# Kernel tuning notes

Hardware: AMD Instinct MI355X
Metric: run time of the kernel (lower is better)

The kernel has to match this reference:

```python
import jax, jax.numpy as jnp
import numpy as np
import math

NUM_WORDS = 8192
WORD_WIDTH = 512
PROJ_WIDTH = 64
NUM_HEADS = 8
SCALE_FACTOR = 100.0

def setup_inputs() -> dict:
    key = jax.random.key(0)
    kx, kq, kk, kv, ko = jax.random.split(key, 5)
    x = jax.random.normal(kx, (NUM_WORDS, WORD_WIDTH), dtype=jnp.float32)
    w_q = jax.random.normal(kq, (WORD_WIDTH, PROJ_WIDTH), dtype=jnp.float32) / SCALE_FACTOR
    w_k = jax.random.normal(kk, (WORD_WIDTH, PROJ_WIDTH), dtype=jnp.float32) / SCALE_FACTOR
    w_v = jax.random.normal(kv, (WORD_WIDTH, PROJ_WIDTH), dtype=jnp.float32) / SCALE_FACTOR
    w_o = jax.random.normal(ko, (WORD_WIDTH, WORD_WIDTH), dtype=jnp.float32)
    return {"x": x, "w_q": w_q, "w_k": w_k, "w_v": w_v, "w_o": w_o}

def reference(x, w_q, w_k, w_v, w_o):
    # Single self-attention head (all 8 heads in the source share the same weights).
    q = x @ w_q            # [N, P]
    k = x @ w_k            # [N, P]
    v = x @ w_v            # [N, P]
    scores = jax.nn.softmax((q @ k.T) / jnp.sqrt(jnp.float32(q.shape[1])), axis=1)  # [N, N]
    head = scores @ v      # [N, P]
    # concat of NUM_HEADS identical head outputs along dim=1
    concat = jnp.tile(head, (1, NUM_HEADS))  # [N, NUM_HEADS*P]
    return concat @ w_o    # [N, WORD_WIDTH]
```

## Files before the change

kernel.cpp:

```cpp
#include <hip/hip_runtime.h>
#include <stdint.h>

#define N_WORDS 8192
#define LOG2E_8 0.18033688011112043f

typedef __attribute__((ext_vector_type(8))) short short8;
typedef __attribute__((ext_vector_type(4))) float f32x4;
typedef __attribute__((ext_vector_type(16))) float f32x16;
typedef __attribute__((ext_vector_type(2))) __fp16 pkhalf2;
typedef __attribute__((ext_vector_type(4))) _Float16 half4;
typedef __attribute__((ext_vector_type(8))) _Float16 half8;

__device__ __forceinline__ unsigned short f32_to_bf16(float f) {
    union { float f; unsigned u; } v; v.f = f;
    unsigned u = v.u;
    return (unsigned short)((u + 0x7FFFu + ((u >> 16) & 1u)) >> 16);
}

__device__ __forceinline__ unsigned short f32_to_f16(float f) {
    union { _Float16 h; unsigned short u; } cv;
    cv.h = (_Float16)f;
    return cv.u;
}

__device__ __forceinline__ void async16(const void* g, void* l) {
    __builtin_amdgcn_global_load_lds(
        (const __attribute__((address_space(1))) unsigned int*)g,
        (__attribute__((address_space(3))) unsigned int*)l, 16, 0, 0);
}

__global__ __launch_bounds__(256) void qkv_gemm(
    const float* __restrict__ x,
    const float* __restrict__ wq, const float* __restrict__ wk,
    const float* __restrict__ wv, const float* __restrict__ wo,
    unsigned short* __restrict__ qB, unsigned short* __restrict__ kB,
    unsigned short* __restrict__ vH, unsigned short* __restrict__ weT)
{
    int t = threadIdx.x;
    int mat = blockIdx.y;

    if (mat == 3) {
        int i = blockIdx.x * 256 + t;
        int p = i >> 9;
        int j = i & 511;
        float s = 0.0f;
#pragma unroll
        for (int h = 0; h < 8; ++h) s += wo[(size_t)(h * 64 + p) * 512 + j];
        weT[(size_t)j * 64 + p] = f32_to_f16(s);
        return;
    }

    __shared__ __align__(16) unsigned short ldsX[64 * 72];
    __shared__ __align__(16) unsigned short ldsW[64 * 72];

    int mt = blockIdx.x;
    const float* w = (mat == 0) ? wq : (mat == 1) ? wk : wv;

    int wvid = t >> 6, lane = t & 63;
    int lq = lane & 15, quad = lane >> 4;

    f32x4 acc[4];
#pragma unroll
    for (int nt = 0; nt < 4; ++nt) acc[nt] = (f32x4){0.f, 0.f, 0.f, 0.f};

    float4 xr[4];
    float wr[16];
    int wn = t & 63, wkbs = (t >> 6) * 16;

    {
#pragma unroll
        for (int j2 = 0; j2 < 4; ++j2) {
            int i = t + j2 * 256;
            int row = i >> 4, c4 = (i & 15) * 4;
            xr[j2] = *(const float4*)(x + (size_t)(mt * 64 + row) * 512 + c4);
        }
#pragma unroll
        for (int kk = 0; kk < 16; ++kk)
            wr[kk] = w[(size_t)(wkbs + kk) * 64 + wn];
    }

    for (int kb = 0; kb < 8; ++kb) {
        __syncthreads();
#pragma unroll
        for (int j2 = 0; j2 < 4; ++j2) {
            int i = t + j2 * 256;
            int row = i >> 4, c4 = (i & 15) * 4;
            unsigned p0 = f32_to_bf16(xr[j2].x) | ((unsigned)f32_to_bf16(xr[j2].y) << 16);
            unsigned p1 = f32_to_bf16(xr[j2].z) | ((unsigned)f32_to_bf16(xr[j2].w) << 16);
            *(uint2*)(&ldsX[row * 72 + c4]) = make_uint2(p0, p1);
        }
#pragma unroll
        for (int kk = 0; kk < 16; kk += 2) {
            unsigned p = f32_to_bf16(wr[kk]) | ((unsigned)f32_to_bf16(wr[kk + 1]) << 16);
            *(unsigned*)(&ldsW[wn * 72 + wkbs + kk]) = p;
        }
        __syncthreads();

        if (kb < 7) {
            int k0 = (kb + 1) * 64;
#pragma unroll
            for (int j2 = 0; j2 < 4; ++j2) {
                int i = t + j2 * 256;
                int row = i >> 4, c4 = (i & 15) * 4;
                xr[j2] = *(const float4*)(x + (size_t)(mt * 64 + row) * 512 + k0 + c4);
            }
#pragma unroll
            for (int kk = 0; kk < 16; ++kk)
                wr[kk] = w[(size_t)(k0 + wkbs + kk) * 64 + wn];
        }

        int m = wvid * 16 + lq;
        short8 a0 = *(const short8*)(&ldsX[m * 72 + quad * 8]);
        short8 a1 = *(const short8*)(&ldsX[m * 72 + 32 + quad * 8]);
#pragma unroll
        for (int nt = 0; nt < 4; ++nt) {
            short8 b0 = *(const short8*)(&ldsW[(nt * 16 + lq) * 72 + quad * 8]);
            short8 b1 = *(const short8*)(&ldsW[(nt * 16 + lq) * 72 + 32 + quad * 8]);
            acc[nt] = __builtin_amdgcn_mfma_f32_16x16x32_bf16(a0, b0, acc[nt], 0, 0, 0);
            acc[nt] = __builtin_amdgcn_mfma_f32_16x16x32_bf16(a1, b1, acc[nt], 0, 0, 0);
        }
    }

    __syncthreads();
    unsigned short* ldsO = ldsX;
#pragma unroll
    for (int nt = 0; nt < 4; ++nt) {
#pragma unroll
        for (int r = 0; r < 4; ++r) {
            int lr = wvid * 16 + quad * 4 + r;
            int n = nt * 16 + lq;
            float v = acc[nt][r];
            int off;
            unsigned short u;
            if (mat == 0) {
                v *= LOG2E_8;
                int col = (((n >> 3) ^ (lr & 7)) << 3) | (n & 7);
                off = lr * 64 + col;
                u = f32_to_bf16(v);
            } else if (mat == 1) {
                int c2 = n >> 3, j = n & 7;
                off = (((lr >> 5) << 2) + (c2 >> 1)) * 512
                    + (((c2 & 1) << 5) + (lr & 31)) * 8 + j;
                u = f32_to_bf16(v);
            } else {
                int j2 = (lr & 3) | (((lr >> 3) & 1) << 2);
                off = ((((lr >> 5) << 1) + ((lr >> 4) & 1)) * 2 + (n >> 5)) * 512
                    + ((((lr >> 2) & 1) << 5) + (n & 31)) * 8 + j2;
                u = f32_to_f16(v);
            }
            ldsO[off] = u;
        }
    }
    __syncthreads();
    {
        unsigned short* dst = (mat == 0) ? qB : (mat == 1) ? kB : vH;
        const uint4* U = (const uint4*)ldsO;
        uint4* G = (uint4*)((char*)dst + (size_t)mt * 8192);
        G[t] = U[t];
        G[t + 256] = U[t + 256];
    }
}

__global__ __launch_bounds__(512, 2) void attn_kernel(
    const unsigned short* __restrict__ qB,
    const unsigned short* __restrict__ kB,
    const unsigned short* __restrict__ vH,
    unsigned short* __restrict__ pOh, float* __restrict__ pl,
    int nk, int sshift)
{
    __shared__ __align__(16) unsigned short ldsK[4][128 * 64];
    __shared__ __align__(16) unsigned short ldsV[4][64 * 128];

    int t = threadIdx.x;
    int bid = blockIdx.x;
    int s = bid & ((1 << sshift) - 1);
    int qb = bid >> sshift;
    int wvid = t >> 6, lane = t & 63;
    int l31 = lane & 31, hi = lane >> 5;
    int mbase = qb * 256 + wvid * 32;
    int n0 = s * nk;

    short8 qf[4];
    {
        int qrow = mbase + l31;
        const unsigned short* qr = qB + (size_t)qrow * 64;
        int s7 = qrow & 7;
#pragma unroll
        for (int c = 0; c < 4; ++c)
            qf[c] = *(const short8*)(qr + (((2 * c + hi) ^ s7) << 3));
    }

    f32x16 zero16;
#pragma unroll
    for (int i = 0; i < 16; ++i) zero16[i] = 0.f;
    f32x16 oacc[2];
    oacc[0] = zero16;
    oacc[1] = zero16;
    float lsum = 0.f;

    auto stage = [&](int ti, int nb) {
        int buf = ti & 3;
        const char* gK = (const char*)kB + (size_t)(nb >> 7) * 16384;
        const char* gV = (const char*)vH + (size_t)(nb >> 7) * 16384;
        async16(gK + ((size_t)(wvid * 64) + lane) * 16,
                (char*)ldsK[buf] + (size_t)wvid * 1024);
        async16(gK + ((size_t)(512 + wvid * 64) + lane) * 16,
                (char*)ldsK[buf] + 8192 + (size_t)wvid * 1024);
        async16(gV + ((size_t)(wvid * 64) + lane) * 16,
                (char*)ldsV[buf] + (size_t)wvid * 1024);
        async16(gV + ((size_t)(512 + wvid * 64) + lane) * 16,
                (char*)ldsV[buf] + 8192 + (size_t)wvid * 1024);
    };

    int tiles = nk >> 7;
    stage(0, n0);
    stage(1, n0 + 128);
    stage(2, n0 + 256);

    for (int tt = 0; tt < tiles; ++tt) {
        int rem = tiles - 1 - tt;
        if (rem >= 2)      asm volatile("s_waitcnt vmcnt(8)" ::: "memory");
        else if (rem == 1) asm volatile("s_waitcnt vmcnt(4)" ::: "memory");
        else               asm volatile("s_waitcnt vmcnt(0)" ::: "memory");
        __builtin_amdgcn_sched_barrier(0);
        __builtin_amdgcn_s_barrier();
        __builtin_amdgcn_sched_barrier(0);

        if (tt + 3 < tiles) stage(tt + 3, n0 + (tt + 3) * 128);

        __builtin_amdgcn_s_setprio(1);
        const char* Kb = (const char*)ldsK[tt & 3] + (size_t)lane * 16;
        const char* Vb = (const char*)ldsV[tt & 3] + (size_t)lane * 16;

#pragma unroll
        for (int nt = 0; nt < 4; ++nt) {
            f32x16 st = zero16;
#pragma unroll
            for (int c = 0; c < 4; ++c) {
                short8 a = *(const short8*)(Kb + (nt * 4 + c) * 1024);
                st = __builtin_amdgcn_mfma_f32_32x32x16_bf16(a, qf[c], st, 0, 0, 0);
            }

            union { half8 v8[2]; pkhalf2 v2[8]; } pa;
#pragma unroll
            for (int p = 0; p < 8; ++p) {
                float e0 = exp2f(st[2 * p]);
                float e1 = exp2f(st[2 * p + 1]);
                lsum += e0 + e1;
                pa.v2[p] = __builtin_amdgcn_cvt_pkrtz(e0, e1);
            }

#pragma unroll
            for (int m = 0; m < 2; ++m) {
#pragma unroll
                for (int vt = 0; vt < 2; ++vt) {
                    half8 vb = *(const half8*)(Vb + (((nt * 2 + m) * 2) + vt) * 1024);
                    oacc[vt] = __builtin_amdgcn_mfma_f32_32x32x16_f16(
                        pa.v8[m], vb, oacc[vt], 0, 0, 0);
                }
            }
        }
        __builtin_amdgcn_s_setprio(0);
    }

    lsum += __shfl_xor(lsum, 32);

    size_t obase = (size_t)s * N_WORDS;
    if (hi == 0) pl[obase + mbase + l31] = lsum;

    __syncthreads();
    unsigned short* ldsO = &ldsK[0][0];
#pragma unroll
    for (int vt = 0; vt < 2; ++vt)
#pragma unroll
        for (int r = 0; r < 16; ++r) {
            int lrow = wvid * 32 + (r & 3) + 8 * (r >> 2) + 4 * hi;
            ldsO[lrow * 64 + vt * 32 + l31] = f32_to_f16(oacc[vt][r]);
        }
    __syncthreads();
    {
        const uint4* U = (const uint4*)ldsO;
        uint4* G = (uint4*)(pOh + (obase + (size_t)qb * 256) * 64);
#pragma unroll
        for (int j = 0; j < 4; ++j)
            G[t + 512 * j] = U[t + 512 * j];
    }
}

__global__ __launch_bounds__(256) void out_kernel(
    const unsigned short* __restrict__ pOh, const float* __restrict__ pl,
    const unsigned short* __restrict__ weT, float* __restrict__ out, int S)
{
    __shared__ __align__(16) _Float16 ldsH[16 * 72];
    int t = threadIdx.x;
    int r0 = blockIdx.x * 16;
    const _Float16* pOf = (const _Float16*)pOh;

#pragma unroll
    for (int j = 0; j < 4; ++j) {
        int i = t + j * 256;
        int row = i >> 6, d = i & 63;
        float so = 0.f, sl = 0.f;
        for (int s = 0; s < S; ++s) {
            so += (float)pOf[((size_t)s * N_WORDS + r0 + row) * 64 + d];
            sl += pl[(size_t)s * N_WORDS + r0 + row];
        }
        ldsH[row * 72 + d] = (_Float16)(so / sl);
    }
    __syncthreads();

    int wv = t >> 6, lane = t & 63;
    int lq = lane & 15, quad = lane >> 4;

    half8 a0 = *(const half8*)(&ldsH[lq * 72 + quad * 8]);
    half8 a1 = *(const half8*)(&ldsH[lq * 72 + 32 + quad * 8]);
    const _Float16* wT = (const _Float16*)weT;

#pragma unroll
    for (int ntl = 0; ntl < 8; ++ntl) {
        int nt = wv * 8 + ntl;
        const _Float16* wrow = wT + (size_t)(nt * 16 + lq) * 64;
        half8 b0 = *(const half8*)(wrow + quad * 8);
        half8 b1 = *(const half8*)(wrow + 32 + quad * 8);
        f32x4 acc = (f32x4){0.f, 0.f, 0.f, 0.f};
        acc = __builtin_amdgcn_mfma_f32_16x16x32_f16(a0, b0, acc, 0, 0, 0);
        acc = __builtin_amdgcn_mfma_f32_16x16x32_f16(a1, b1, acc, 0, 0, 0);
#pragma unroll
        for (int r = 0; r < 4; ++r)
            out[(size_t)(r0 + quad * 4 + r) * 512 + nt * 16 + lq] = acc[r];
    }
}

extern "C" void kernel_launch(void* const* d_in, const int* in_sizes, int n_in,
                              void* d_out, int out_size, void* d_ws, size_t ws_size,
                              hipStream_t stream)
{
    const float* x  = (const float*)d_in[0];
    const float* wq = (const float*)d_in[1];
    const float* wk = (const float*)d_in[2];
    const float* wv = (const float*)d_in[3];
    const float* wo = (const float*)d_in[4];
    float* out = (float*)d_out;

    char* ws = (char*)d_ws;
    unsigned short* qB  = (unsigned short*)(ws);
    unsigned short* kB  = (unsigned short*)(ws + 1048576);
    unsigned short* vH  = (unsigned short*)(ws + 2097152);
    unsigned short* weT = (unsigned short*)(ws + 3145728);
    float* pl           = (float*)(ws + 3211264);
    unsigned short* pOh = (unsigned short*)(ws + 3735552);

    size_t base = 3735552;
    int S = (ws_size >= base + 8u * 1048576u) ? 8 : 4;
    int sshift = (S == 8) ? 3 : 2;
    int nk = N_WORDS / S;
    int nqb = N_WORDS / 256;

    hipLaunchKernelGGL(qkv_gemm, dim3(128, 4), dim3(256), 0, stream,
                       x, wq, wk, wv, wo, qB, kB, vH, weT);
    hipLaunchKernelGGL(attn_kernel, dim3(nqb * S), dim3(512), 0, stream,
                       qB, kB, vH, pOh, pl, nk, sshift);
    hipLaunchKernelGGL(out_kernel, dim3(512), dim3(256), 0, stream,
                       pOh, pl, weT, out, S);
}
```

Baseline: 124.9 us.

## Fuse Q/K/V projections per block with 16-row tiles across 512 blocks

The QKV projection kernel now computes all three projections in one block over a 16-row tile of x, so each x tile is loaded and converted once instead of three times. The grid becomes 512 one-dimensional blocks instead of 128x4, and the w_o head-sum reduction is folded into the first 64 threads of each block. Output layouts are rewritten so the K and V tiled formats still match what the attention kernel expects. In exchange, every block reloads all three weight matrices, which raises weight traffic and register use.

```diff
diff --git a/kernel.cpp b/kernel.cpp
--- a/kernel.cpp
+++ b/kernel.cpp
@@ -36,100 +36,79 @@
     unsigned short* __restrict__ qB, unsigned short* __restrict__ kB,
     unsigned short* __restrict__ vH, unsigned short* __restrict__ weT)
 {
+    __shared__ __align__(16) unsigned short ldsX[16 * 72];
+    __shared__ __align__(16) unsigned short ldsW[3][64 * 72];
+
     int t = threadIdx.x;
-    int mat = blockIdx.y;
-
-    if (mat == 3) {
-        int i = blockIdx.x * 256 + t;
-        int p = i >> 9;
-        int j = i & 511;
-        float s = 0.0f;
-#pragma unroll
-        for (int h = 0; h < 8; ++h) s += wo[(size_t)(h * 64 + p) * 512 + j];
-        weT[(size_t)j * 64 + p] = f32_to_f16(s);
-        return;
-    }
-
-    __shared__ __align__(16) unsigned short ldsX[64 * 72];
-    __shared__ __align__(16) unsigned short ldsW[64 * 72];
-
     int mt = blockIdx.x;
-    const float* w = (mat == 0) ? wq : (mat == 1) ? wk : wv;
+    const float* wmat[3] = {wq, wk, wv};
 
     int wvid = t >> 6, lane = t & 63;
     int lq = lane & 15, quad = lane >> 4;
 
-    f32x4 acc[4];
-#pragma unroll
-    for (int nt = 0; nt < 4; ++nt) acc[nt] = (f32x4){0.f, 0.f, 0.f, 0.f};
-
-    float4 xr[4];
-    float wr[16];
+    f32x4 acc[3];
+#pragma unroll
+    for (int mat = 0; mat < 3; ++mat) acc[mat] = (f32x4){0.f, 0.f, 0.f, 0.f};
+
+    float4 xr;
+    float wr[3][16];
+    int xrow = t >> 4, xc4 = (t & 15) * 4;
     int wn = t & 63, wkbs = (t >> 6) * 16;
 
-    {
-#pragma unroll
-        for (int j2 = 0; j2 < 4; ++j2) {
-            int i = t + j2 * 256;
-            int row = i >> 4, c4 = (i & 15) * 4;
-            xr[j2] = *(const float4*)(x + (size_t)(mt * 64 + row) * 512 + c4);
-        }
+    xr = *(const float4*)(x + (size_t)(mt * 16 + xrow) * 512 + xc4);
+#pragma unroll
+    for (int mat = 0; mat < 3; ++mat)
 #pragma unroll
         for (int kk = 0; kk < 16; ++kk)
-            wr[kk] = w[(size_t)(wkbs + kk) * 64 + wn];
-    }
+            wr[mat][kk] = wmat[mat][(size_t)(wkbs + kk) * 64 + wn];
 
     for (int kb = 0; kb < 8; ++kb) {
         __syncthreads();
-#pragma unroll
-        for (int j2 = 0; j2 < 4; ++j2) {
-            int i = t + j2 * 256;
-            int row = i >> 4, c4 = (i & 15) * 4;
-            unsigned p0 = f32_to_bf16(xr[j2].x) | ((unsigned)f32_to_bf16(xr[j2].y) << 16);
-            unsigned p1 = f32_to_bf16(xr[j2].z) | ((unsigned)f32_to_bf16(xr[j2].w) << 16);
-            *(uint2*)(&ldsX[row * 72 + c4]) = make_uint2(p0, p1);
-        }
-#pragma unroll
-        for (int kk = 0; kk < 16; kk += 2) {
-            unsigned p = f32_to_bf16(wr[kk]) | ((unsigned)f32_to_bf16(wr[kk + 1]) << 16);
-            *(unsigned*)(&ldsW[wn * 72 + wkbs + kk]) = p;
-        }
+        {
+            unsigned p0 = f32_to_bf16(xr.x) | ((unsigned)f32_to_bf16(xr.y) << 16);
+            unsigned p1 = f32_to_bf16(xr.z) | ((unsigned)f32_to_bf16(xr.w) << 16);
+            *(uint2*)(&ldsX[xrow * 72 + xc4]) = make_uint2(p0, p1);
+        }
+#pragma unroll
+        for (int mat = 0; mat < 3; ++mat)
+#pragma unroll
+            for (int kk = 0; kk < 16; kk += 2) {
+                unsigned p = f32_to_bf16(wr[mat][kk]) |
+                             ((unsigned)f32_to_bf16(wr[mat][kk + 1]) << 16);
+                *(unsigned*)(&ldsW[mat][wn * 72 + wkbs + kk]) = p;
+            }
         __syncthreads();
 
         if (kb < 7) {
             int k0 = (kb + 1) * 64;
-#pragma unroll
-            for (int j2 = 0; j2 < 4; ++j2) {
-                int i = t + j2 * 256;
-                int row = i >> 4, c4 = (i & 15) * 4;
-                xr[j2] = *(const float4*)(x + (size_t)(mt * 64 + row) * 512 + k0 + c4);
-            }
-#pragma unroll
-            for (int kk = 0; kk < 16; ++kk)
-                wr[kk] = w[(size_t)(k0 + wkbs + kk) * 64 + wn];
-        }
-
-        int m = wvid * 16 + lq;
-        short8 a0 = *(const short8*)(&ldsX[m * 72 + quad * 8]);
-        short8 a1 = *(const short8*)(&ldsX[m * 72 + 32 + quad * 8]);
-#pragma unroll
-        for (int nt = 0; nt < 4; ++nt) {
-            short8 b0 = *(const short8*)(&ldsW[(nt * 16 + lq) * 72 + quad * 8]);
-            short8 b1 = *(const short8*)(&ldsW[(nt * 16 + lq) * 72 + 32 + quad * 8]);
-            acc[nt] = __builtin_amdgcn_mfma_f32_16x16x32_bf16(a0, b0, acc[nt], 0, 0, 0);
-            acc[nt] = __builtin_amdgcn_mfma_f32_16x16x32_bf16(a1, b1, acc[nt], 0, 0, 0);
-        }
-    }
-
-    __syncthreads();
-    unsigned short* ldsO = ldsX;
-#pragma unroll
-    for (int nt = 0; nt < 4; ++nt) {
+            xr = *(const float4*)(x + (size_t)(mt * 16 + xrow) * 512 + k0 + xc4);
+#pragma unroll
+            for (int mat = 0; mat < 3; ++mat)
+#pragma unroll
+                for (int kk = 0; kk < 16; ++kk)
+                    wr[mat][kk] = wmat[mat][(size_t)(k0 + wkbs + kk) * 64 + wn];
+        }
+
+        short8 a0 = *(const short8*)(&ldsX[lq * 72 + quad * 8]);
+        short8 a1 = *(const short8*)(&ldsX[lq * 72 + 32 + quad * 8]);
+#pragma unroll
+        for (int mat = 0; mat < 3; ++mat) {
+            short8 b0 = *(const short8*)(&ldsW[mat][(wvid * 16 + lq) * 72 + quad * 8]);
+            short8 b1 = *(const short8*)(&ldsW[mat][(wvid * 16 + lq) * 72 + 32 + quad * 8]);
+            acc[mat] = __builtin_amdgcn_mfma_f32_16x16x32_bf16(a0, b0, acc[mat], 0, 0, 0);
+            acc[mat] = __builtin_amdgcn_mfma_f32_16x16x32_bf16(a1, b1, acc[mat], 0, 0, 0);
+        }
+    }
+
+    __syncthreads();
+    unsigned short* ldsO = &ldsW[0][0];
+#pragma unroll
+    for (int mat = 0; mat < 3; ++mat) {
 #pragma unroll
         for (int r = 0; r < 4; ++r) {
-            int lr = wvid * 16 + quad * 4 + r;
-            int n = nt * 16 + lq;
-            float v = acc[nt][r];
+            int lr = quad * 4 + r;
+            int n = wvid * 16 + lq;
+            float v = acc[mat][r];
             int off;
             unsigned short u;
             if (mat == 0) {
@@ -139,13 +118,13 @@
                 u = f32_to_bf16(v);
             } else if (mat == 1) {
                 int c2 = n >> 3, j = n & 7;
-                off = (((lr >> 5) << 2) + (c2 >> 1)) * 512
-                    + (((c2 & 1) << 5) + (lr & 31)) * 8 + j;
+                off = 1024 + c2 * 128 + lr * 8 + j;
                 u = f32_to_bf16(v);
             } else {
                 int j2 = (lr & 3) | (((lr >> 3) & 1) << 2);
-                off = ((((lr >> 5) << 1) + ((lr >> 4) & 1)) * 2 + (n >> 5)) * 512
-                    + ((((lr >> 2) & 1) << 5) + (n & 31)) * 8 + j2;
+                int hi2 = (lr >> 2) & 1;
+                int vt = n >> 5;
+                off = 2048 + vt * 512 + ((hi2 << 5) + (n & 31)) * 8 + j2;
                 u = f32_to_f16(v);
             }
             ldsO[off] = u;
@@ -153,11 +132,26 @@
     }
     __syncthreads();
     {
-        unsigned short* dst = (mat == 0) ? qB : (mat == 1) ? kB : vH;
         const uint4* U = (const uint4*)ldsO;
-        uint4* G = (uint4*)((char*)dst + (size_t)mt * 8192);
-        G[t] = U[t];
-        G[t + 256] = U[t + 256];
+        if (t < 128) {
+            ((uint4*)qB)[(size_t)mt * 128 + t] = U[t];
+            ((uint4*)vH)[(size_t)mt * 128 + t] = U[256 + t];
+        } else {
+            int tt = t - 128;
+            int c2 = tt >> 4, idx = tt & 15;
+            ((uint4*)kB)[(size_t)(mt >> 1) * 256 + (c2 >> 1) * 64 +
+                         (c2 & 1) * 32 + (mt & 1) * 16 + idx] = U[128 + c2 * 16 + idx];
+        }
+    }
+
+    if (t < 64) {
+        int i = mt * 64 + t;
+        int p = i >> 9;
+        int j = i & 511;
+        float s = 0.0f;
+#pragma unroll
+        for (int h = 0; h < 8; ++h) s += wo[(size_t)(h * 64 + p) * 512 + j];
+        weT[(size_t)j * 64 + p] = f32_to_f16(s);
     }
 }
 
@@ -356,7 +350,7 @@
     int nk = N_WORDS / S;
     int nqb = N_WORDS / 256;
 
-    hipLaunchKernelGGL(qkv_gemm, dim3(128, 4), dim3(256), 0, stream,
+    hipLaunchKernelGGL(qkv_gemm, dim3(512), dim3(256), 0, stream,
                        x, wq, wk, wv, wo, qB, kB, vH, weT);
     hipLaunchKernelGGL(attn_kernel, dim3(nqb * S), dim3(512), 0, stream,
                        qB, kB, vH, pOh, pl, nk, sshift);
```

New measurement: 128.6 us. 2.9% more time.
